# Optimization experiments

Hardware: AMD Instinct MI355X
Metric: run time of the kernel (lower is better)

Reference implementation:

```python
import jax, jax.numpy as jnp
import numpy as np

B, W, E, D, F = 128, 64, 256, 256, 4  # batch, window, enc_hidden, dec_hidden, out_feats


def setup_inputs() -> dict:
    key = jax.random.key(0)
    ks = jax.random.split(key, 16)
    s = 0.05
    return {
        "input_encoded": jax.random.normal(ks[0], (B, W, E), jnp.float32),
        "y_history": jax.random.normal(ks[1], (B, W, F), jnp.float32),
        # attn_layer: Linear(2D+E -> E), Tanh, Linear(E -> 1)
        "attn_w1": jax.random.normal(ks[2], (E, 2 * D + E), jnp.float32) * s,
        "attn_b1": jax.random.normal(ks[3], (E,), jnp.float32) * s,
        "attn_w2": jax.random.normal(ks[4], (1, E), jnp.float32) * s,
        "attn_b2": jax.random.normal(ks[5], (1,), jnp.float32) * s,
        # single-layer LSTM cell: input F, hidden D (gate order i,f,g,o)
        "w_ih": jax.random.normal(ks[6], (4 * D, F), jnp.float32) * s,
        "w_hh": jax.random.normal(ks[7], (4 * D, D), jnp.float32) * s,
        "b_ih": jax.random.normal(ks[8], (4 * D,), jnp.float32) * s,
        "b_hh": jax.random.normal(ks[9], (4 * D,), jnp.float32) * s,
        # fc: Linear(E+F -> F) (weights normal_() in torch, scaled here for stability)
        "fc_w": jax.random.normal(ks[10], (F, E + F), jnp.float32) * s,
        "fc_b": jax.random.normal(ks[11], (F,), jnp.float32) * s,
        # fc_final: Linear(D+E -> F)
        "fcf_w": jax.random.normal(ks[12], (F, D + E), jnp.float32) * s,
        "fcf_b": jax.random.normal(ks[13], (F,), jnp.float32) * s,
    }


def _decoder(input_encoded, y_history, attn_w1, attn_b1, attn_w2, attn_b2,
             w_ih, w_hh, b_ih, b_hh, fc_w, fc_b, fcf_w, fcf_b):
    b = input_encoded.shape[0]
    h0 = jnp.zeros((b, D), input_encoded.dtype)
    c0 = jnp.zeros((b, D), input_encoded.dtype)
    ctx0 = jnp.zeros((b, E), input_encoded.dtype)
    y_seq = jnp.transpose(y_history, (1, 0, 2))  # [W, B, F]

    def step(carry, y_t):
        h, c, _ = carry  # h, c: [B, D]
        # additive attention over encoder timesteps
        hc = jnp.broadcast_to(h[:, None, :], (b, W, D))
        cc = jnp.broadcast_to(c[:, None, :], (b, W, D))
        x = jnp.concatenate([hc, cc, input_encoded], axis=2)  # [B, W, 2D+E]
        z = jnp.tanh(jnp.einsum('bwk,ek->bwe', x, attn_w1) + attn_b1)
        scores = jnp.einsum('bwe,oe->bwo', z, attn_w2)[..., 0] + attn_b2[0]  # [B, W]
        attn = jax.nn.softmax(scores, axis=1)
        context = jnp.einsum('bw,bwe->be', attn, input_encoded)  # [B, E]
        # fc over (context, y_t)
        y_tilde = jnp.concatenate([context, y_t], axis=1) @ fc_w.T + fc_b  # [B, F]
        # one LSTM cell step (torch gate order: i, f, g, o)
        gates = y_tilde @ w_ih.T + b_ih + h @ w_hh.T + b_hh  # [B, 4D]
        i_g, f_g, g_g, o_g = jnp.split(gates, 4, axis=1)
        c_new = jax.nn.sigmoid(f_g) * c + jax.nn.sigmoid(i_g) * jnp.tanh(g_g)
        h_new = jax.nn.sigmoid(o_g) * jnp.tanh(c_new)
        return (h_new, c_new, context), None

    (h, c, context), _ = jax.lax.scan(step, (h0, c0, ctx0), y_seq)
    return jnp.concatenate([h, context], axis=1) @ fcf_w.T + fcf_b  # [B, F]


def reference(input_encoded, y_history, attn_w1, attn_b1, attn_w2, attn_b2,
              w_ih, w_hh, b_ih, b_hh, fc_w, fc_b, fcf_w, fcf_b):
    return _decoder(input_encoded, y_history, attn_w1, attn_b1, attn_w2, attn_b2,
                    w_ih, w_hh, b_ih, b_hh, fc_w, fc_b, fcf_w, fcf_b)
```

## Files before the change

kernel.cpp:

```cpp
#include <hip/hip_runtime.h>

#define Bn 128
#define Wn 64

typedef _Float16 h2 __attribute__((ext_vector_type(2)));

__device__ unsigned g_sf[256];
__device__ unsigned g_stf[256];
__device__ unsigned g_scp[256][2][256];
__device__ unsigned g_stp[256][2][128];
__device__ unsigned g_ep16[Bn * Wn * 128];
__device__ float4 g_encfc[Bn * Wn];
__device__ float4 g_encfcf[Bn * Wn];
__device__ uint4 g_w1pk[8 * 32 * 64];
__device__ uint4 g_whpk[8 * 128 * 32];

__device__ __forceinline__ float ftanh(float x) {
  float p = __builtin_exp2f(x * 2.885390081777927f);
  return 1.0f - 2.0f * __builtin_amdgcn_rcpf(p + 1.0f);
}
__device__ __forceinline__ float fsigm(float x) {
  float p = __builtin_exp2f(-x * 1.4426950408889634f);
  return __builtin_amdgcn_rcpf(1.0f + p);
}
__device__ __forceinline__ float dot4(float4 a, float4 b) {
  return a.x * b.x + a.y * b.y + a.z * b.z + a.w * b.w;
}
__device__ __forceinline__ float fd2(unsigned w, unsigned h, float acc) {
  h2 a = __builtin_bit_cast(h2, w), b = __builtin_bit_cast(h2, h);
#if __has_builtin(__builtin_amdgcn_fdot2)
  return __builtin_amdgcn_fdot2(a, b, acc, false);
#else
  return acc + (float)a.x * (float)b.x + (float)a.y * (float)b.y;
#endif
}
__device__ __forceinline__ float fd2x4u(uint4 w, uint4 h, float acc) {
  acc = fd2(w.x, h.x, acc);
  acc = fd2(w.y, h.y, acc);
  acc = fd2(w.z, h.z, acc);
  acc = fd2(w.w, h.w, acc);
  return acc;
}
__device__ __forceinline__ unsigned pk(float a, float b) {
  h2 h = {(_Float16)a, (_Float16)b};
  return __builtin_bit_cast(unsigned, h);
}
__device__ __forceinline__ void ast(unsigned* p, unsigned v) {
  __hip_atomic_store(p, v, __ATOMIC_RELAXED, __HIP_MEMORY_SCOPE_AGENT);
}
__device__ __forceinline__ unsigned ald(unsigned* p) {
  return __hip_atomic_load(p, __ATOMIC_RELAXED, __HIP_MEMORY_SCOPE_AGENT);
}
__device__ __forceinline__ float aldf(unsigned* p) {
  return __builtin_bit_cast(float, ald(p));
}

#define STPHYS(c, L) ((c) * 68 + ((L) >> 4) * 17 + ((L) & 15))

__global__ void reset_kernel(float* out) {
  int t = threadIdx.x;
  if (t < 256) { g_sf[t] = 0u; g_stf[t] = 0u; }
  if (t < 512) out[t] = 0.f;
}

__global__ __launch_bounds__(256) void pack_kernel(const float* __restrict__ w1,
                                                   const float* __restrict__ w_hh) {
  int idx = blockIdx.x * 256 + threadIdx.x;
  const float* src;
  uint4* dst;
  if (idx < 16384) {
    int m = idx >> 11, e_loc = (idx >> 6) & 31, ku = idx & 63;
    int e = m * 32 + e_loc;
    src = w1 + (size_t)e * 768 + 8 * ku;
    dst = g_w1pk + idx;
  } else {
    int j = idx - 16384;
    int m = j >> 12, rq = (j >> 5) & 127, i = j & 31;
    int q = rq >> 5, dl = rq & 31;
    int R = q * 256 + m * 32 + dl;
    src = w_hh + (size_t)R * 256 + 8 * i;
    dst = g_whpk + j;
  }
  uint4 o;
  o.x = pk(src[0], src[1]); o.y = pk(src[2], src[3]);
  o.z = pk(src[4], src[5]); o.w = pk(src[6], src[7]);
  *dst = o;
}

__global__ __launch_bounds__(256) void eproj_kernel(const float* __restrict__ enc,
                                                    const float* __restrict__ w1,
                                                    const float* __restrict__ b1) {
  __shared__ __align__(16) float4 encs[16][64];
  __shared__ float accs[16][256];
  const int m0 = blockIdx.x * 16;
  const int tid = threadIdx.x;
  const float4* eg = (const float4*)(enc + (size_t)m0 * 256);
#pragma unroll
  for (int i = 0; i < 4; i++) {
    int idx = tid + 256 * i;
    encs[idx >> 6][idx & 63] = eg[idx];
  }
  __syncthreads();
  const int e = tid;
  float acc[16];
#pragma unroll
  for (int i = 0; i < 16; i++) acc[i] = 0.f;
  const float4* wrow = (const float4*)(w1 + e * 768 + 512);
  for (int k4 = 0; k4 < 64; k4++) {
    float4 wv = wrow[k4];
#pragma unroll
    for (int i = 0; i < 16; i++) acc[i] += dot4(wv, encs[i][k4]);
  }
  float bb = b1[e];
#pragma unroll
  for (int i = 0; i < 16; i++) accs[i][e] = acc[i] + bb;
  __syncthreads();
#pragma unroll
  for (int r = 0; r < 8; r++) {
    int idx = r * 256 + tid;
    int i = idx >> 7, jp = idx & 127;
    g_ep16[(size_t)(m0 + i) * 128 + jp] = pk(accs[i][2 * jp], accs[i][2 * jp + 1]);
  }
}

__global__ __launch_bounds__(256) void encfc_kernel(const float* __restrict__ enc,
                                                    const float* __restrict__ fc_w,
                                                    const float* __restrict__ fcf_w) {
  __shared__ __align__(16) float4 encs[16][64];
  const int m0 = blockIdx.x * 16;
  const int tid = threadIdx.x;
  const float4* eg = (const float4*)(enc + (size_t)m0 * 256);
#pragma unroll
  for (int i = 0; i < 4; i++) {
    int idx = tid + 256 * i;
    encs[idx >> 6][idx & 63] = eg[idx];
  }
  __syncthreads();
  if (tid < 128) {
    const int r = tid >> 3, o = tid & 7;
    const float* wr = (o < 4) ? (fc_w + o * 260) : (fcf_w + (o - 4) * 512 + 256);
    const float4* w4 = (const float4*)wr;
    float a = 0.f;
#pragma unroll 8
    for (int k = 0; k < 64; k++) a += dot4(w4[k], encs[r][k]);
    if (o < 4) ((float*)&g_encfc[m0 + r])[o] = a;
    else ((float*)&g_encfcf[m0 + r])[o - 4] = a;
  }
}

__global__ __launch_bounds__(512, 1) void decoder_kernel(
    const float* __restrict__ yhist, const float* __restrict__ w2,
    const float* __restrict__ w_ih, const float* __restrict__ b_ih,
    const float* __restrict__ b_hh,
    const float* __restrict__ fc_w, const float* __restrict__ fc_b,
    const float* __restrict__ fcf_w, const float* __restrict__ fcf_b,
    float* __restrict__ out) {
  __shared__ __align__(16) uint4 w1l[32 * 65];
  __shared__ __align__(16) uint4 whl[128 * 33];
  __shared__ __align__(16) uint4 ep_t[4 * 257];
  __shared__ __align__(16) uint4 st4[4 * 68];
  __shared__ __align__(16) float4 encfc_l[256];
  __shared__ __align__(16) float4 yh_l[256];
  __shared__ __align__(16) float4 wihl[132];
  __shared__ float biasl[132];
  __shared__ float ag_l[4 * 133];
  __shared__ float hcp_l[4 * 36];
  __shared__ float w2_l[32];
  __shared__ float scp_l[256];
  __shared__ float sc_part[7 * 256];
  __shared__ float cl[132];
  __shared__ __align__(16) float4 ytl[4];
  __shared__ float fcy_l[16];
  __shared__ float fcb_l[4];

  const int g = blockIdx.x, t = threadIdx.x;
  const int m = (g >> 3) & 7;
  const int gx = g - 8 * m;
  const int G = (g & 7) * 4 + (g >> 6);
  const int cbase = 4 * G;
  const int l = t & 63, wv = t >> 6;
  const int e_loc = t >> 4, ks = t & 15;
  const int row = t >> 2, kq2 = t & 3;

  unsigned* st32 = (unsigned*)st4;

#pragma unroll
  for (int j = 0; j < 4; j++) {
    int f = t + 512 * j;
    w1l[(f >> 6) * 65 + (f & 63)] = g_w1pk[m * 2048 + f];
  }
#pragma unroll
  for (int j = 0; j < 8; j++) {
    int f = t + 512 * j;
    whl[(f >> 5) * 33 + (f & 31)] = g_whpk[m * 4096 + f];
  }
#pragma unroll
  for (int j = 0; j < 2; j++) {
    int f = t + 512 * j;
    int u = f >> 8, cw = f & 255, c = cw >> 6, w = cw & 63;
    ep_t[u * 257 + cw] =
        ((const uint4*)(g_ep16 + ((size_t)((cbase + c) * 64 + w)) * 128))[m * 4 + u];
  }
  if (t < 272) st4[t] = (uint4){0u, 0u, 0u, 0u};
  if (t < 256) {
    int c = t >> 6, w = t & 63;
    encfc_l[t] = g_encfc[(cbase + c) * 64 + w];
    yh_l[t] = ((const float4*)yhist)[(cbase + c) * 64 + w];
  }
  if (t < 128) {
    int q = t >> 5, dl = t & 31;
    int R = q * 256 + m * 32 + dl;
    wihl[q * 33 + dl] = *(const float4*)(w_ih + (size_t)R * 4);
    biasl[q * 33 + dl] = b_ih[R] + b_hh[R];
  }
  if (t < 132) cl[t] = 0.f;
  if (t < 32) w2_l[t] = w2[m * 32 + t];
  if (t < 16) fcy_l[t] = fc_w[(t >> 2) * 260 + 256 + (t & 3)];
  if (t < 4) fcb_l[t] = fc_b[t];
  __syncthreads();

  float attw = 0.f;
  for (int tstep = 0; tstep < Wn; tstep++) {
    const int tb = tstep & 1;
    const unsigned want = (unsigned)(tstep + 1);
    {
      float a0 = 0.f, a1 = 0.f, a2 = 0.f, a3 = 0.f;
      const uint4* wrow = &w1l[e_loc * 65 + 4 * ks];
#pragma unroll
      for (int j = 0; j < 4; j++) {
        uint4 wvv = wrow[j];
        int ku = 4 * ks + j;
        int ph = (ku >> 4) * 17 + (ku & 15);
        a0 = fd2x4u(wvv, st4[ph], a0);
        a1 = fd2x4u(wvv, st4[68 + ph], a1);
        a2 = fd2x4u(wvv, st4[136 + ph], a2);
        a3 = fd2x4u(wvv, st4[204 + ph], a3);
      }
#pragma unroll
      for (int dd = 1; dd < 16; dd <<= 1) {
        a0 += __shfl_xor(a0, dd, 64);
        a1 += __shfl_xor(a1, dd, 64);
        a2 += __shfl_xor(a2, dd, 64);
        a3 += __shfl_xor(a3, dd, 64);
      }
      if (ks == 0) {
        hcp_l[e_loc] = a0;
        hcp_l[36 + e_loc] = a1;
        hcp_l[72 + e_loc] = a2;
        hcp_l[108 + e_loc] = a3;
      }
    }
    __syncthreads();
    {
      const int cB = t >> 7, wB = (t & 127) >> 1, halfB = t & 1;
      float s = 0.f;
#pragma unroll
      for (int j = 0; j < 2; j++) {
        int u = 2 * halfB + j;
        uint4 uu = ep_t[u * 257 + cB * 64 + wB];
        unsigned um[4] = {uu.x, uu.y, uu.z, uu.w};
#pragma unroll
        for (int ui = 0; ui < 4; ui++) {
          int e0 = 2 * (4 * u + ui);
          h2 aa = __builtin_bit_cast(h2, um[ui]);
          s += w2_l[e0] * ftanh((float)aa.x + hcp_l[cB * 36 + e0]);
          s += w2_l[e0 + 1] * ftanh((float)aa.y + hcp_l[cB * 36 + e0 + 1]);
        }
      }
      s += __shfl_xor(s, 1, 64);
      if (halfB == 0) scp_l[cB * 64 + wB] = s;
    }
    __syncthreads();
    if (wv == 0) {
      unsigned* dst = &g_scp[g][tb][4 * l];
      ast(dst + 0, __builtin_bit_cast(unsigned, scp_l[4 * l + 0]));
      ast(dst + 1, __builtin_bit_cast(unsigned, scp_l[4 * l + 1]));
      ast(dst + 2, __builtin_bit_cast(unsigned, scp_l[4 * l + 2]));
      ast(dst + 3, __builtin_bit_cast(unsigned, scp_l[4 * l + 3]));
      asm volatile("s_waitcnt vmcnt(0)" ::: "memory");
      if (l == 0) ast(&g_sf[g], want);
    }
    {
      float b0 = 0.f, b1 = 0.f, b2 = 0.f, b3 = 0.f;
      const uint4* wr = &whl[row * 33 + 8 * kq2];
#pragma unroll
      for (int j = 0; j < 8; j++) {
        uint4 wvv = wr[j];
        int i = 8 * kq2 + j;
        int ph = (i >> 4) * 17 + (i & 15);
        b0 = fd2x4u(wvv, st4[ph], b0);
        b1 = fd2x4u(wvv, st4[68 + ph], b1);
        b2 = fd2x4u(wvv, st4[136 + ph], b2);
        b3 = fd2x4u(wvv, st4[204 + ph], b3);
      }
#pragma unroll
      for (int dd = 1; dd < 4; dd <<= 1) {
        b0 += __shfl_xor(b0, dd, 64);
        b1 += __shfl_xor(b1, dd, 64);
        b2 += __shfl_xor(b2, dd, 64);
        b3 += __shfl_xor(b3, dd, 64);
      }
      if (kq2 == 0) {
        ag_l[row] = b0;
        ag_l[133 + row] = b1;
        ag_l[266 + row] = b2;
        ag_l[399 + row] = b3;
      }
    }
    if (wv >= 1) {
      const int mo = (m + wv) & 7;
      if (l == 0) {
        unsigned* fp = &g_sf[gx + 8 * mo];
        while (ald(fp) < want) __builtin_amdgcn_s_sleep(1);
      }
      asm volatile("" ::: "memory");
      unsigned* sp = &g_scp[gx + 8 * mo][tb][4 * l];
      float* dst = &sc_part[(wv - 1) * 256 + 4 * l];
      dst[0] = aldf(sp + 0);
      dst[1] = aldf(sp + 1);
      dst[2] = aldf(sp + 2);
      dst[3] = aldf(sp + 3);
    }
    __syncthreads();
    if (wv < 4) {
      const int c = wv;
      float sc = scp_l[c * 64 + l];
#pragma unroll
      for (int k = 0; k < 7; k++) sc += sc_part[k * 256 + c * 64 + l];
      float mm = sc;
#pragma unroll
      for (int dd = 32; dd; dd >>= 1) mm = fmaxf(mm, __shfl_xor(mm, dd, 64));
      float pr = __builtin_exp2f((sc - mm) * 1.4426950408889634f);
      float su = pr;
#pragma unroll
      for (int dd = 32; dd; dd >>= 1) su += __shfl_xor(su, dd, 64);
      attw = pr * __builtin_amdgcn_rcpf(su);
      float4 ef = encfc_l[c * 64 + l];
      float rx = attw * ef.x, ry = attw * ef.y, rz = attw * ef.z, rw = attw * ef.w;
#pragma unroll
      for (int dd = 32; dd; dd >>= 1) {
        rx += __shfl_xor(rx, dd, 64);
        ry += __shfl_xor(ry, dd, 64);
        rz += __shfl_xor(rz, dd, 64);
        rw += __shfl_xor(rw, dd, 64);
      }
      if (l == 0) {
        float4 yv = yh_l[c * 64 + tstep];
        float4 yt;
        yt.x = rx + fcb_l[0] + fcy_l[0] * yv.x + fcy_l[1] * yv.y + fcy_l[2] * yv.z + fcy_l[3] * yv.w;
        yt.y = ry + fcb_l[1] + fcy_l[4] * yv.x + fcy_l[5] * yv.y + fcy_l[6] * yv.z + fcy_l[7] * yv.w;
        yt.z = rz + fcb_l[2] + fcy_l[8] * yv.x + fcy_l[9] * yv.y + fcy_l[10] * yv.z + fcy_l[11] * yv.w;
        yt.w = rw + fcb_l[3] + fcy_l[12] * yv.x + fcy_l[13] * yv.y + fcy_l[14] * yv.z + fcy_l[15] * yv.w;
        ytl[c] = yt;
      }
    }
    __syncthreads();
    if (wv == 0) {
      const int c = l >> 4, pp = l & 15;
      const int d0 = 2 * pp, d1 = d0 + 1;
      float4 yt = ytl[c];
#define GV(q, d) (ag_l[c * 133 + (q) * 32 + (d)] + biasl[(q) * 33 + (d)] + dot4(wihl[(q) * 33 + (d)], yt))
      float i0 = fsigm(GV(0, d0)), f0 = fsigm(GV(1, d0));
      float G0 = ftanh(GV(2, d0)), o0 = fsigm(GV(3, d0));
      float i1 = fsigm(GV(0, d1)), f1 = fsigm(GV(1, d1));
      float G1 = ftanh(GV(2, d1)), o1 = fsigm(GV(3, d1));
#undef GV
      float cn0 = f0 * cl[c * 33 + d0] + i0 * G0;
      float cn1 = f1 * cl[c * 33 + d1] + i1 * G1;
      float hn0 = o0 * ftanh(cn0), hn1 = o1 * ftanh(cn1);
      cl[c * 33 + d0] = cn0; cl[c * 33 + d1] = cn1;
      unsigned hp = pk(hn0, hn1), cp = pk(cn0, cn1);
      {
        int Lh = 4 * m + (pp >> 2), Lc = 32 + 4 * m + (pp >> 2);
        st32[4 * STPHYS(c, Lh) + (pp & 3)] = hp;
        st32[4 * STPHYS(c, Lc) + (pp & 3)] = cp;
      }
      if (tstep < 63) {
        ast(&g_stp[g][tb][c * 32 + pp], hp);
        ast(&g_stp[g][tb][c * 32 + 16 + pp], cp);
        asm volatile("s_waitcnt vmcnt(0)" ::: "memory");
        if (l == 0) ast(&g_stf[g], want);
      }
    } else if (tstep < 63) {
      const int mo = (m + wv) & 7;
      if (l == 0) {
        unsigned* fp = &g_stf[gx + 8 * mo];
        while (ald(fp) < want) __builtin_amdgcn_s_sleep(1);
      }
      asm volatile("" ::: "memory");
      if (l < 32) {
        unsigned* sp = &g_stp[gx + 8 * mo][tb][4 * l];
#pragma unroll
        for (int k2 = 0; k2 < 4; k2++) {
          unsigned v = ald(sp + k2);
          int i = 4 * l + k2;
          int c = i >> 5, r = i & 31, pp = r & 15, isC = r >> 4;
          int L = isC * 32 + 4 * mo + (pp >> 2);
          st32[4 * STPHYS(c, L) + (pp & 3)] = v;
        }
      }
    }
    __syncthreads();
  }

  if (wv < 4) {
    const int c = wv, b = cbase + c;
    const int pp = l & 15, f = l >> 4;
    int Lh = 4 * m + (pp >> 2);
    h2 hh = __builtin_bit_cast(h2, st32[4 * STPHYS(c, Lh) + (pp & 3)]);
    const int d0 = m * 32 + 2 * pp;
    float v = fcf_w[f * 512 + d0] * (float)hh.x + fcf_w[f * 512 + d0 + 1] * (float)hh.y;
#pragma unroll
    for (int dd = 1; dd < 16; dd <<= 1) v += __shfl_xor(v, dd, 64);
    if (pp == 0) atomicAdd(out + b * 4 + f, v);
    if (m == 0) {
      float4 fv = g_encfcf[b * 64 + l];
      float vx = attw * fv.x, vy = attw * fv.y, vz = attw * fv.z, vw = attw * fv.w;
#pragma unroll
      for (int dd = 32; dd; dd >>= 1) {
        vx += __shfl_xor(vx, dd, 64);
        vy += __shfl_xor(vy, dd, 64);
        vz += __shfl_xor(vz, dd, 64);
        vw += __shfl_xor(vw, dd, 64);
      }
      if (l == 0) {
        atomicAdd(out + b * 4 + 0, vx + fcf_b[0]);
        atomicAdd(out + b * 4 + 1, vy + fcf_b[1]);
        atomicAdd(out + b * 4 + 2, vz + fcf_b[2]);
        atomicAdd(out + b * 4 + 3, vw + fcf_b[3]);
      }
    }
  }
}

extern "C" void kernel_launch(void* const* d_in, const int* in_sizes, int n_in,
                              void* d_out, int out_size, void* d_ws, size_t ws_size,
                              hipStream_t stream) {
  (void)in_sizes; (void)n_in; (void)d_ws; (void)ws_size; (void)out_size;
  const float* enc   = (const float*)d_in[0];
  const float* yhist = (const float*)d_in[1];
  const float* w1    = (const float*)d_in[2];
  const float* b1    = (const float*)d_in[3];
  const float* w2    = (const float*)d_in[4];
  const float* w_ih  = (const float*)d_in[6];
  const float* w_hh  = (const float*)d_in[7];
  const float* b_ih  = (const float*)d_in[8];
  const float* b_hh  = (const float*)d_in[9];
  const float* fc_w  = (const float*)d_in[10];
  const float* fc_b  = (const float*)d_in[11];
  const float* fcf_w = (const float*)d_in[12];
  const float* fcf_b = (const float*)d_in[13];
  float* out = (float*)d_out;

  reset_kernel<<<dim3(1), dim3(512), 0, stream>>>(out);
  pack_kernel<<<dim3(192), dim3(256), 0, stream>>>(w1, w_hh);
  eproj_kernel<<<dim3(512), dim3(256), 0, stream>>>(enc, w1, b1);
  encfc_kernel<<<dim3(512), dim3(256), 0, stream>>>(enc, fc_w, fcf_w);
  decoder_kernel<<<dim3(256), dim3(512), 0, stream>>>(yhist, w2, w_ih, b_ih, b_hh,
                                                      fc_w, fc_b, fcf_w, fcf_b, out);
}
```

Measured before the change: 600.6 us.

## Double decoder block size to 1024 threads and halve per-thread work

Launches the persistent decoder kernel with 1024 threads per block instead of 512 and reassigns the per-step matvecs (attention hidden projection, recurrent gate matvec, tanh-score reduction) so each thread handles half as many elements, with one extra shuffle-reduction level each. The extra waves stay out of the cross-block flag polling. The yt staging buffer now lives in padding slots of the gate accumulator array. The aim is to cut per-step latency of the sequential recurrence. In exchange it adds register pressure under the 1024-thread bound, more shuffle steps, and larger barriers per step.

```diff
diff --git a/kernel.cpp b/kernel.cpp
--- a/kernel.cpp
+++ b/kernel.cpp
@@ -148,7 +148,7 @@
   }
 }
 
-__global__ __launch_bounds__(512, 1) void decoder_kernel(
+__global__ __launch_bounds__(1024, 1) void decoder_kernel(
     const float* __restrict__ yhist, const float* __restrict__ w2,
     const float* __restrict__ w_ih, const float* __restrict__ b_ih,
     const float* __restrict__ b_hh,
@@ -169,7 +169,6 @@
   __shared__ float scp_l[256];
   __shared__ float sc_part[7 * 256];
   __shared__ float cl[132];
-  __shared__ __align__(16) float4 ytl[4];
   __shared__ float fcy_l[16];
   __shared__ float fcb_l[4];
 
@@ -179,24 +178,23 @@
   const int G = (g & 7) * 4 + (g >> 6);
   const int cbase = 4 * G;
   const int l = t & 63, wv = t >> 6;
-  const int e_loc = t >> 4, ks = t & 15;
-  const int row = t >> 2, kq2 = t & 3;
+  const int e_loc = t >> 5, ks5 = t & 31;
+  const int row = t >> 3, kq3 = t & 7;
 
   unsigned* st32 = (unsigned*)st4;
 
 #pragma unroll
+  for (int j = 0; j < 2; j++) {
+    int f = t + 1024 * j;
+    w1l[(f >> 6) * 65 + (f & 63)] = g_w1pk[m * 2048 + f];
+  }
+#pragma unroll
   for (int j = 0; j < 4; j++) {
-    int f = t + 512 * j;
-    w1l[(f >> 6) * 65 + (f & 63)] = g_w1pk[m * 2048 + f];
-  }
-#pragma unroll
-  for (int j = 0; j < 8; j++) {
-    int f = t + 512 * j;
+    int f = t + 1024 * j;
     whl[(f >> 5) * 33 + (f & 31)] = g_whpk[m * 4096 + f];
   }
-#pragma unroll
-  for (int j = 0; j < 2; j++) {
-    int f = t + 512 * j;
+  {
+    int f = t;
     int u = f >> 8, cw = f & 255, c = cw >> 6, w = cw & 63;
     ep_t[u * 257 + cw] =
         ((const uint4*)(g_ep16 + ((size_t)((cbase + c) * 64 + w)) * 128))[m * 4 + u];
@@ -225,11 +223,11 @@
     const unsigned want = (unsigned)(tstep + 1);
     {
       float a0 = 0.f, a1 = 0.f, a2 = 0.f, a3 = 0.f;
-      const uint4* wrow = &w1l[e_loc * 65 + 4 * ks];
-#pragma unroll
-      for (int j = 0; j < 4; j++) {
+      const uint4* wrow = &w1l[e_loc * 65 + 2 * ks5];
+#pragma unroll
+      for (int j = 0; j < 2; j++) {
         uint4 wvv = wrow[j];
-        int ku = 4 * ks + j;
+        int ku = 2 * ks5 + j;
         int ph = (ku >> 4) * 17 + (ku & 15);
         a0 = fd2x4u(wvv, st4[ph], a0);
         a1 = fd2x4u(wvv, st4[68 + ph], a1);
@@ -237,13 +235,13 @@
         a3 = fd2x4u(wvv, st4[204 + ph], a3);
       }
 #pragma unroll
-      for (int dd = 1; dd < 16; dd <<= 1) {
+      for (int dd = 1; dd < 32; dd <<= 1) {
         a0 += __shfl_xor(a0, dd, 64);
         a1 += __shfl_xor(a1, dd, 64);
         a2 += __shfl_xor(a2, dd, 64);
         a3 += __shfl_xor(a3, dd, 64);
       }
-      if (ks == 0) {
+      if (ks5 == 0) {
         hcp_l[e_loc] = a0;
         hcp_l[36 + e_loc] = a1;
         hcp_l[72 + e_loc] = a2;
@@ -252,23 +250,20 @@
     }
     __syncthreads();
     {
-      const int cB = t >> 7, wB = (t & 127) >> 1, halfB = t & 1;
+      const int cB = t >> 8, wB = (t >> 2) & 63, qB = t & 3;
       float s = 0.f;
-#pragma unroll
-      for (int j = 0; j < 2; j++) {
-        int u = 2 * halfB + j;
-        uint4 uu = ep_t[u * 257 + cB * 64 + wB];
-        unsigned um[4] = {uu.x, uu.y, uu.z, uu.w};
-#pragma unroll
-        for (int ui = 0; ui < 4; ui++) {
-          int e0 = 2 * (4 * u + ui);
-          h2 aa = __builtin_bit_cast(h2, um[ui]);
-          s += w2_l[e0] * ftanh((float)aa.x + hcp_l[cB * 36 + e0]);
-          s += w2_l[e0 + 1] * ftanh((float)aa.y + hcp_l[cB * 36 + e0 + 1]);
-        }
+      uint4 uu = ep_t[qB * 257 + cB * 64 + wB];
+      unsigned um[4] = {uu.x, uu.y, uu.z, uu.w};
+#pragma unroll
+      for (int ui = 0; ui < 4; ui++) {
+        int e0 = 2 * (4 * qB + ui);
+        h2 aa = __builtin_bit_cast(h2, um[ui]);
+        s += w2_l[e0] * ftanh((float)aa.x + hcp_l[cB * 36 + e0]);
+        s += w2_l[e0 + 1] * ftanh((float)aa.y + hcp_l[cB * 36 + e0 + 1]);
       }
       s += __shfl_xor(s, 1, 64);
-      if (halfB == 0) scp_l[cB * 64 + wB] = s;
+      s += __shfl_xor(s, 2, 64);
+      if (qB == 0) scp_l[cB * 64 + wB] = s;
     }
     __syncthreads();
     if (wv == 0) {
@@ -282,11 +277,11 @@
     }
     {
       float b0 = 0.f, b1 = 0.f, b2 = 0.f, b3 = 0.f;
-      const uint4* wr = &whl[row * 33 + 8 * kq2];
-#pragma unroll
-      for (int j = 0; j < 8; j++) {
+      const uint4* wr = &whl[row * 33 + 4 * kq3];
+#pragma unroll
+      for (int j = 0; j < 4; j++) {
         uint4 wvv = wr[j];
-        int i = 8 * kq2 + j;
+        int i = 4 * kq3 + j;
         int ph = (i >> 4) * 17 + (i & 15);
         b0 = fd2x4u(wvv, st4[ph], b0);
         b1 = fd2x4u(wvv, st4[68 + ph], b1);
@@ -294,20 +289,20 @@
         b3 = fd2x4u(wvv, st4[204 + ph], b3);
       }
 #pragma unroll
-      for (int dd = 1; dd < 4; dd <<= 1) {
+      for (int dd = 1; dd < 8; dd <<= 1) {
         b0 += __shfl_xor(b0, dd, 64);
         b1 += __shfl_xor(b1, dd, 64);
         b2 += __shfl_xor(b2, dd, 64);
         b3 += __shfl_xor(b3, dd, 64);
       }
-      if (kq2 == 0) {
+      if (kq3 == 0) {
         ag_l[row] = b0;
         ag_l[133 + row] = b1;
         ag_l[266 + row] = b2;
         ag_l[399 + row] = b3;
       }
     }
-    if (wv >= 1) {
+    if (wv >= 1 && wv <= 7) {
       const int mo = (m + wv) & 7;
       if (l == 0) {
         unsigned* fp = &g_sf[gx + 8 * mo];
@@ -351,14 +346,14 @@
         yt.y = ry + fcb_l[1] + fcy_l[4] * yv.x + fcy_l[5] * yv.y + fcy_l[6] * yv.z + fcy_l[7] * yv.w;
         yt.z = rz + fcb_l[2] + fcy_l[8] * yv.x + fcy_l[9] * yv.y + fcy_l[10] * yv.z + fcy_l[11] * yv.w;
         yt.w = rw + fcb_l[3] + fcy_l[12] * yv.x + fcy_l[13] * yv.y + fcy_l[14] * yv.z + fcy_l[15] * yv.w;
-        ytl[c] = yt;
+        *(float4*)&ag_l[c * 133 + 128] = yt;
       }
     }
     __syncthreads();
     if (wv == 0) {
       const int c = l >> 4, pp = l & 15;
       const int d0 = 2 * pp, d1 = d0 + 1;
-      float4 yt = ytl[c];
+      float4 yt = *(const float4*)&ag_l[c * 133 + 128];
 #define GV(q, d) (ag_l[c * 133 + (q) * 32 + (d)] + biasl[(q) * 33 + (d)] + dot4(wihl[(q) * 33 + (d)], yt))
       float i0 = fsigm(GV(0, d0)), f0 = fsigm(GV(1, d0));
       float G0 = ftanh(GV(2, d0)), o0 = fsigm(GV(3, d0));
@@ -381,7 +376,7 @@
         asm volatile("s_waitcnt vmcnt(0)" ::: "memory");
         if (l == 0) ast(&g_stf[g], want);
       }
-    } else if (tstep < 63) {
+    } else if (wv <= 7 && tstep < 63) {
       const int mo = (m + wv) & 7;
       if (l == 0) {
         unsigned* fp = &g_stf[gx + 8 * mo];
@@ -456,6 +451,6 @@
   pack_kernel<<<dim3(192), dim3(256), 0, stream>>>(w1, w_hh);
   eproj_kernel<<<dim3(512), dim3(256), 0, stream>>>(enc, w1, b1);
   encfc_kernel<<<dim3(512), dim3(256), 0, stream>>>(enc, fc_w, fcf_w);
-  decoder_kernel<<<dim3(256), dim3(512), 0, stream>>>(yhist, w2, w_ih, b_ih, b_hh,
-                                                      fc_w, fc_b, fcf_w, fcf_b, out);
-}
+  decoder_kernel<<<dim3(256), dim3(1024), 0, stream>>>(yhist, w2, w_ih, b_ih, b_hh,
+                                                       fc_w, fc_b, fcf_w, fcf_b, out);
+}
```

Result: slower. 703.2 us (+17.1%).
